# Optimization experiments

Hardware: AMD Instinct MI355X
Metric: run time of the kernel (lower is better)

The kernel has to match this reference:

```python
import jax, jax.numpy as jnp
import numpy as np


def _simple_rnn(x_tbd, Wx, Wh, b, return_sequences):
    # x_tbd: [T, B, D]; h_t = tanh(x_t @ Wx + h_{t-1} @ Wh + b)
    B = x_tbd.shape[1]
    H = Wh.shape[0]
    # precompute input projection for all steps (single big GEMM)
    xw = jnp.einsum('tbd,dh->tbh', x_tbd, Wx) + b

    def step(h, xw_t):
        h_new = jnp.tanh(xw_t + h @ Wh)
        return h_new, h_new if return_sequences else None

    h0 = jnp.zeros((B, H), dtype=x_tbd.dtype)
    h_last, hs = jax.lax.scan(step, h0, xw)
    return hs if return_sequences else h_last


def setup_inputs() -> dict:
    key = jax.random.key(0)
    ks = jax.random.split(key, 8)
    B, T, D, H, C = 32, 1024, 128, 512, 10
    s_in = 1.0 / np.sqrt(D)
    s_h = 1.0 / np.sqrt(H)
    return {
        'x': jax.random.normal(ks[0], (B, T, D), jnp.float32),
        'Wx1': jax.random.normal(ks[1], (D, H), jnp.float32) * s_in,
        'Wh1': jax.random.normal(ks[2], (H, H), jnp.float32) * s_h,
        'b1': jnp.zeros((H,), jnp.float32),
        'Wx2': jax.random.normal(ks[3], (H, H), jnp.float32) * s_h,
        'Wh2': jax.random.normal(ks[4], (H, H), jnp.float32) * s_h,
        'b2': jnp.zeros((H,), jnp.float32),
        'Wo': jax.random.normal(ks[5], (H, C), jnp.float32) * s_h,
        'bo': jnp.zeros((C,), jnp.float32),
    }


def reference(x, Wx1, Wh1, b1, Wx2, Wh2, b2, Wo, bo):
    # x: [B, T, D] -> time-major [T, B, D]
    x_t = jnp.swapaxes(x, 0, 1)
    h1 = _simple_rnn(x_t, Wx1, Wh1, b1, return_sequences=True)   # [T, B, H]
    h2 = _simple_rnn(h1, Wx2, Wh2, b2, return_sequences=False)   # [B, H]
    logits = h2 @ Wo + bo
    return jax.nn.softmax(logits, axis=-1)
```

## Files before the change

### kernel.cpp

```cpp
#include <hip/hip_runtime.h>
#include <hip/hip_fp16.h>
#include <math.h>

#define BATCH 32
#define TLEN  1024
#define DIN   128
#define HID   512
#define NCLS  10
#define NB    2
#define NGRP  (BATCH/NB)
#define NSL   8
#define RING  32
#define SENTV 0xFFFFFFFFu
#define POLL_CAP (1u<<17)

typedef _Float16 hf2 __attribute__((ext_vector_type(2)));

__device__ __forceinline__ unsigned aload(const unsigned* p) {
  return __hip_atomic_load(p, __ATOMIC_RELAXED, __HIP_MEMORY_SCOPE_AGENT);
}
__device__ __forceinline__ void astore(unsigned* p, unsigned v) {
  __hip_atomic_store(p, v, __ATOMIC_RELAXED, __HIP_MEMORY_SCOPE_AGENT);
}
__device__ __forceinline__ int aloadi(const int* p) {
  return __hip_atomic_load(p, __ATOMIC_RELAXED, __HIP_MEMORY_SCOPE_AGENT);
}
__device__ __forceinline__ void astorei(int* p, int v) {
  __hip_atomic_store(p, v, __ATOMIC_RELAXED, __HIP_MEMORY_SCOPE_AGENT);
}

__device__ __forceinline__ float fdot2u(unsigned a, unsigned b, float c) {
#if __has_builtin(__builtin_amdgcn_fdot2)
  return __builtin_amdgcn_fdot2(__builtin_bit_cast(hf2, a),
                                __builtin_bit_cast(hf2, b), c, false);
#else
  hf2 av = __builtin_bit_cast(hf2, a), bv = __builtin_bit_cast(hf2, b);
  return c + (float)av[0] * (float)bv[0] + (float)av[1] * (float)bv[1];
#endif
}

__device__ __forceinline__ unsigned packh2(float lo, float hi) {
  __half2 h = __floats2half2_rn(lo, hi);
  return __builtin_bit_cast(unsigned, h);
}

__global__ __launch_bounds__(256) void k_xw1(
    const float* __restrict__ x, const float* __restrict__ Wx1,
    const float* __restrict__ b1, unsigned* __restrict__ xw1)
{
  __shared__ float xst[DIN * 4];
  const int tid  = threadIdx.x;
  const int row0 = blockIdx.x * 4;
  for (int idx = tid; idx < 4 * DIN; idx += 256) {
    int r = idx >> 7, d = idx & (DIN - 1);
    int row = row0 + r;
    int t = row >> 5, b = row & 31;
    xst[d * 4 + r] = x[((size_t)b * TLEN + t) * DIN + d];
  }
  __syncthreads();
  float acc[4][2];
#pragma unroll
  for (int r = 0; r < 4; ++r) { acc[r][0] = 0.f; acc[r][1] = 0.f; }
  const int j0 = 2 * tid, j1 = 2 * tid + 1;
  for (int d = 0; d < DIN; ++d) {
    float w0 = Wx1[(size_t)d * HID + j0];
    float w1 = Wx1[(size_t)d * HID + j1];
    float4 xv = *reinterpret_cast<const float4*>(&xst[d * 4]);
    acc[0][0] += xv.x * w0; acc[0][1] += xv.x * w1;
    acc[1][0] += xv.y * w0; acc[1][1] += xv.y * w1;
    acc[2][0] += xv.z * w0; acc[2][1] += xv.z * w1;
    acc[3][0] += xv.w * w0; acc[3][1] += xv.w * w1;
  }
  float bb0 = b1[j0], bb1 = b1[j1];
#pragma unroll
  for (int r = 0; r < 4; ++r)
    xw1[(size_t)(row0 + r) * 256 + tid] = packh2(acc[r][0] + bb0, acc[r][1] + bb1);
}

__global__ __launch_bounds__(512, 2) void k_rnn(
    const unsigned* __restrict__ xw1,
    const float* __restrict__ Wh1,
    const float* __restrict__ Wx2, const float* __restrict__ Wh2,
    const float* __restrict__ b2,
    unsigned* __restrict__ ringA,
    unsigned* __restrict__ ringB,
    unsigned* __restrict__ ringC,
    int* __restrict__ prog2,
    float* __restrict__ h2fin)
{
  const int tid  = threadIdx.x;
  const int wgid = blockIdx.x;
  const int layer = wgid >> 7;
  const int lw = wgid & 127;
  const int g  = lw >> 3, sl = lw & 7;
  const int b0 = g * NB;
  const int c0 = sl * 64;
  const int w  = tid >> 6, j = tid & 63;
  const int col = c0 + j;

  __shared__ __align__(16) unsigned h_s[NB][512];
  __shared__ float red[8][NB][64];

  if (layer == 0) {
    const int kw = w * 32;
    unsigned wreg[32];
    {
      const int k0 = w * 64;
#pragma unroll
      for (int i = 0; i < 32; ++i) {
        float a = Wh1[(size_t)(k0 + 2 * i) * HID + col];
        float b = Wh1[(size_t)(k0 + 2 * i + 1) * HID + col];
        wreg[i] = packh2(a, b);
      }
    }
    int cached = -1;
    const int pb = tid >> 8;
    const int pw = tid & 255;
    for (int t = 0; t < TLEN; ++t) {
      unsigned xww = 0;
      if (tid < 128) {
        int bb = tid >> 6, jj = tid & 63;
        xww = xw1[((size_t)t * BATCH + b0 + bb) * 256 + ((c0 + jj) >> 1)];
      }
      if (w < 2) {
        int need = t - (RING - 6);
        if (cached < need) {
          unsigned it = 0;
          for (;;) {
            int p = (j < NSL) ? aloadi(&prog2[g * NSL + j]) : 0x7fffffff;
#pragma unroll
            for (int d = 1; d < NSL; d <<= 1) p = min(p, __shfl_xor(p, d));
            p = __shfl(p, 0);
            cached = p;
            if (cached >= need || ++it >= POLL_CAP) break;
          }
        }
      }
      {
        unsigned v = 0;
        if (t > 0) {
          const unsigned* p =
              &ringA[((size_t)((t - 1) & (RING - 1)) * BATCH + b0 + pb) * 256 + pw];
          unsigned it = 0;
          do { v = aload(p); } while (v == SENTV && ++it < POLL_CAP);
          if (v == SENTV) v = 0;
        }
        h_s[pb][pw] = v;
      }
      if (tid < 64) {
        int bb = tid >> 5, wi = (c0 >> 1) + (tid & 31);
        size_t off = ((size_t)((t + 1) & (RING - 1)) * BATCH + b0 + bb) * 256 + wi;
        astore(&ringA[off], SENTV);
        astore(&ringB[off], SENTV);
      }
      __syncthreads();
      float acc0 = 0.f, acc1 = 0.f;
#pragma unroll
      for (int i = 0; i < 8; ++i) {
        uint4 ha = *reinterpret_cast<const uint4*>(&h_s[0][kw + 4 * i]);
        uint4 hb = *reinterpret_cast<const uint4*>(&h_s[1][kw + 4 * i]);
        acc0 = fdot2u(ha.x, wreg[4 * i + 0], acc0);
        acc0 = fdot2u(ha.y, wreg[4 * i + 1], acc0);
        acc0 = fdot2u(ha.z, wreg[4 * i + 2], acc0);
        acc0 = fdot2u(ha.w, wreg[4 * i + 3], acc0);
        acc1 = fdot2u(hb.x, wreg[4 * i + 0], acc1);
        acc1 = fdot2u(hb.y, wreg[4 * i + 1], acc1);
        acc1 = fdot2u(hb.z, wreg[4 * i + 2], acc1);
        acc1 = fdot2u(hb.w, wreg[4 * i + 3], acc1);
      }
      red[w][0][j] = acc0;
      red[w][1][j] = acc1;
      __syncthreads();
      if (tid < 128) {
        int bb = tid >> 6, jj = tid & 63;
        hf2 xv = __builtin_bit_cast(hf2, xww);
        float z = (float)xv[jj & 1];
#pragma unroll
        for (int r = 0; r < 8; ++r) z += red[r][bb][jj];
        float h = tanhf(z);
        float hn = __shfl_down(h, 1);
        if ((jj & 1) == 0) {
          unsigned u = packh2(h, hn);
          size_t off = ((size_t)(t & (RING - 1)) * BATCH + b0 + bb) * 256 + ((c0 + jj) >> 1);
          astore(&ringA[off], u);
          astore(&ringB[off], u);
        }
      }
    }
  } else {
    const int kw = w * 64;
    unsigned wreg[64];
    {
      const int k0 = w * 128;
#pragma unroll
      for (int i = 0; i < 64; ++i) {
        int k = k0 + 2 * i;
        float a, b;
        if (k < HID) {
          a = Wx2[(size_t)k * HID + col];
          b = Wx2[(size_t)(k + 1) * HID + col];
        } else {
          a = Wh2[(size_t)(k - HID) * HID + col];
          b = Wh2[(size_t)(k - HID + 1) * HID + col];
        }
        wreg[i] = packh2(a, b);
      }
    }
    float b2v = 0.f;
    if (tid < 128) b2v = b2[c0 + (tid & 63)];
    for (int t = 0; t < TLEN; ++t) {
      {
        const unsigned* p0 = nullptr; const unsigned* p1 = nullptr;
        unsigned v0 = 0, v1 = 0;
        if (tid < 256) {
          size_t base = ((size_t)(t & (RING - 1)) * BATCH + b0) * 256 + tid;
          p0 = &ringB[base]; p1 = &ringB[base + 256];
          v0 = SENTV; v1 = SENTV;
        } else if (t > 0) {
          size_t base = ((size_t)((t - 1) & (RING - 1)) * BATCH + b0) * 256 + (tid - 256);
          p0 = &ringC[base]; p1 = &ringC[base + 256];
          v0 = SENTV; v1 = SENTV;
        }
        if (p0) {
          unsigned it = 0;
          while ((v0 == SENTV || v1 == SENTV) && it < POLL_CAP) {
            if (v0 == SENTV) v0 = aload(p0);
            if (v1 == SENTV) v1 = aload(p1);
            ++it;
          }
          if (v0 == SENTV) v0 = 0;
          if (v1 == SENTV) v1 = 0;
        }
        h_s[0][tid] = v0;
        h_s[1][tid] = v1;
      }
      if (tid < 64) {
        int bb = tid >> 5, wi = (c0 >> 1) + (tid & 31);
        astore(&ringC[((size_t)((t + 1) & (RING - 1)) * BATCH + b0 + bb) * 256 + wi], SENTV);
      }
      __syncthreads();
      if (tid == 0) astorei(&prog2[g * NSL + sl], t);
      float acc0 = 0.f, acc1 = 0.f;
#pragma unroll
      for (int i = 0; i < 16; ++i) {
        uint4 ha = *reinterpret_cast<const uint4*>(&h_s[0][kw + 4 * i]);
        uint4 hb = *reinterpret_cast<const uint4*>(&h_s[1][kw + 4 * i]);
        acc0 = fdot2u(ha.x, wreg[4 * i + 0], acc0);
        acc0 = fdot2u(ha.y, wreg[4 * i + 1], acc0);
        acc0 = fdot2u(ha.z, wreg[4 * i + 2], acc0);
        acc0 = fdot2u(ha.w, wreg[4 * i + 3], acc0);
        acc1 = fdot2u(hb.x, wreg[4 * i + 0], acc1);
        acc1 = fdot2u(hb.y, wreg[4 * i + 1], acc1);
        acc1 = fdot2u(hb.z, wreg[4 * i + 2], acc1);
        acc1 = fdot2u(hb.w, wreg[4 * i + 3], acc1);
      }
      red[w][0][j] = acc0;
      red[w][1][j] = acc1;
      __syncthreads();
      if (tid < 128) {
        int bb = tid >> 6, jj = tid & 63;
        float z = b2v;
#pragma unroll
        for (int r = 0; r < 8; ++r) z += red[r][bb][jj];
        float h = tanhf(z);
        if (t == TLEN - 1) h2fin[(size_t)(b0 + bb) * HID + c0 + jj] = h;
        float hn = __shfl_down(h, 1);
        if ((jj & 1) == 0) {
          astore(&ringC[((size_t)(t & (RING - 1)) * BATCH + b0 + bb) * 256 + ((c0 + jj) >> 1)],
                 packh2(h, hn));
        }
      }
    }
  }
}

__global__ __launch_bounds__(640) void k_head(
    const float* __restrict__ h2, const float* __restrict__ Wo,
    const float* __restrict__ bo, float* __restrict__ out)
{
  __shared__ float lg[16];
  const int b = blockIdx.x;
  const int c = threadIdx.x >> 6;
  const int l = threadIdx.x & 63;
  float p = 0.f;
#pragma unroll
  for (int i = 0; i < 8; ++i) {
    int k = l + 64 * i;
    p += h2[(size_t)b * HID + k] * Wo[(size_t)k * NCLS + c];
  }
  for (int off = 32; off; off >>= 1) p += __shfl_down(p, off);
  if (l == 0) lg[c] = p + bo[c];
  __syncthreads();
  if (threadIdx.x == 0) {
    float m = lg[0];
    for (int i = 1; i < NCLS; ++i) m = fmaxf(m, lg[i]);
    float e[NCLS];
    float s = 0.f;
    for (int i = 0; i < NCLS; ++i) { e[i] = expf(lg[i] - m); s += e[i]; }
    for (int i = 0; i < NCLS; ++i) out[(size_t)b * NCLS + i] = e[i] / s;
  }
}

extern "C" void kernel_launch(void* const* d_in, const int* in_sizes, int n_in,
                              void* d_out, int out_size, void* d_ws, size_t ws_size,
                              hipStream_t stream)
{
  (void)in_sizes; (void)n_in; (void)out_size; (void)ws_size;
  const float* x   = (const float*)d_in[0];
  const float* Wx1 = (const float*)d_in[1];
  const float* Wh1 = (const float*)d_in[2];
  const float* b1  = (const float*)d_in[3];
  const float* Wx2 = (const float*)d_in[4];
  const float* Wh2 = (const float*)d_in[5];
  const float* b2  = (const float*)d_in[6];
  const float* Wo  = (const float*)d_in[7];
  const float* bo  = (const float*)d_in[8];
  float* out = (float*)d_out;

  char* ws = (char*)d_ws;
  size_t o = 0;
  unsigned* xw1 = (unsigned*)(ws + o); o += (size_t)TLEN * BATCH * 256 * 4;
  const size_t ringBytes = (size_t)RING * BATCH * 256 * 4;
  unsigned* ringA = (unsigned*)(ws + o); o += ringBytes;
  unsigned* ringB = (unsigned*)(ws + o); o += ringBytes;
  unsigned* ringC = (unsigned*)(ws + o); o += ringBytes;
  int* prog2 = (int*)(ws + o); o += 1024;
  float* h2fin = (float*)(ws + o); o += (size_t)BATCH * HID * 4;

  hipMemsetAsync(ringA, 0xFF, 3 * ringBytes, stream);
  hipMemsetAsync(prog2, 0xFF, NGRP * NSL * 4, stream);

  k_xw1<<<TLEN * BATCH / 4, 256, 0, stream>>>(x, Wx1, b1, xw1);
  k_rnn<<<256, 512, 0, stream>>>(xw1, Wh1, Wx2, Wh2, b2,
                                 ringA, ringB, ringC, prog2, h2fin);
  k_head<<<BATCH, 640, 0, stream>>>(h2fin, Wo, bo, out);
}
```

Baseline: 2.445 ms.

## Reduce partial sums via wave shuffles and double-buffer shared hidden state

Each wave now owns 16 output columns of one batch row. Four lane-quarters split the K dimension and are combined with cross-lane shuffles, which removes the shared-memory reduction array and the second barrier per timestep. The shared hidden-state buffer is double-buffered by step parity so one barrier per step is enough. The duplicate layer-1 ring is merged into one buffer read by both layers. Weight registers per thread double, and the occupancy hint in the launch bounds is dropped, which raises register pressure.

```diff
diff --git a/kernel.cpp b/kernel.cpp
--- a/kernel.cpp
+++ b/kernel.cpp
@@ -77,13 +77,12 @@
     xw1[(size_t)(row0 + r) * 256 + tid] = packh2(acc[r][0] + bb0, acc[r][1] + bb1);
 }
 
-__global__ __launch_bounds__(512, 2) void k_rnn(
+__global__ __launch_bounds__(512) void k_rnn(
     const unsigned* __restrict__ xw1,
     const float* __restrict__ Wh1,
     const float* __restrict__ Wx2, const float* __restrict__ Wh2,
     const float* __restrict__ b2,
-    unsigned* __restrict__ ringA,
-    unsigned* __restrict__ ringB,
+    unsigned* __restrict__ ring1,
     unsigned* __restrict__ ringC,
     int* __restrict__ prog2,
     float* __restrict__ h2fin)
@@ -95,180 +94,152 @@
   const int g  = lw >> 3, sl = lw & 7;
   const int b0 = g * NB;
   const int c0 = sl * 64;
-  const int w  = tid >> 6, j = tid & 63;
-  const int col = c0 + j;
-
-  __shared__ __align__(16) unsigned h_s[NB][512];
-  __shared__ float red[8][NB][64];
+  const int w  = tid >> 6, l = tid & 63;
+  const int q  = l >> 4;
+  const int lo = l & 15;
+  const int o  = w * 16 + lo;
+  const int obb = o >> 6, oj = o & 63;
+  const int ocol = c0 + oj;
+
+  const int pw = tid & 255;
+  const int pb = tid >> 8;
+
+  __shared__ __align__(16) unsigned h_s[2][NB][512];
 
   if (layer == 0) {
-    const int kw = w * 32;
-    unsigned wreg[32];
+    unsigned wreg[64];
     {
-      const int k0 = w * 64;
-#pragma unroll
-      for (int i = 0; i < 32; ++i) {
-        float a = Wh1[(size_t)(k0 + 2 * i) * HID + col];
-        float b = Wh1[(size_t)(k0 + 2 * i + 1) * HID + col];
+      const int k0 = q * 128;
+#pragma unroll
+      for (int i = 0; i < 64; ++i) {
+        float a = Wh1[(size_t)(k0 + 2 * i) * HID + ocol];
+        float b = Wh1[(size_t)(k0 + 2 * i + 1) * HID + ocol];
         wreg[i] = packh2(a, b);
       }
     }
     int cached = -1;
-    const int pb = tid >> 8;
-    const int pw = tid & 255;
     for (int t = 0; t < TLEN; ++t) {
+      const int p = t & 1;
       unsigned xww = 0;
-      if (tid < 128) {
-        int bb = tid >> 6, jj = tid & 63;
-        xww = xw1[((size_t)t * BATCH + b0 + bb) * 256 + ((c0 + jj) >> 1)];
-      }
-      if (w < 2) {
-        int need = t - (RING - 6);
+      if (q == 0)
+        xww = xw1[((size_t)t * BATCH + b0 + obb) * 256 + (ocol >> 1)];
+      if (w == 0) {
+        const int need = t - (RING - 6);
         if (cached < need) {
           unsigned it = 0;
           for (;;) {
-            int p = (j < NSL) ? aloadi(&prog2[g * NSL + j]) : 0x7fffffff;
-#pragma unroll
-            for (int d = 1; d < NSL; d <<= 1) p = min(p, __shfl_xor(p, d));
-            p = __shfl(p, 0);
-            cached = p;
+            int pr = (l < NSL) ? aloadi(&prog2[g * NSL + l]) : 0x7fffffff;
+#pragma unroll
+            for (int d = 1; d < NSL; d <<= 1) pr = min(pr, __shfl_xor(pr, d));
+            pr = __shfl(pr, 0);
+            cached = pr;
             if (cached >= need || ++it >= POLL_CAP) break;
           }
         }
+        int rb = l >> 5, rw = (c0 >> 1) + (l & 31);
+        astore(&ring1[((size_t)((t + 1) & (RING - 1)) * BATCH + b0 + rb) * 256 + rw], SENTV);
       }
       {
         unsigned v = 0;
         if (t > 0) {
-          const unsigned* p =
-              &ringA[((size_t)((t - 1) & (RING - 1)) * BATCH + b0 + pb) * 256 + pw];
+          const unsigned* pp =
+              &ring1[((size_t)((t - 1) & (RING - 1)) * BATCH + b0 + pb) * 256 + pw];
           unsigned it = 0;
-          do { v = aload(p); } while (v == SENTV && ++it < POLL_CAP);
+          do { v = aload(pp); } while (v == SENTV && ++it < POLL_CAP);
           if (v == SENTV) v = 0;
         }
-        h_s[pb][pw] = v;
-      }
-      if (tid < 64) {
-        int bb = tid >> 5, wi = (c0 >> 1) + (tid & 31);
-        size_t off = ((size_t)((t + 1) & (RING - 1)) * BATCH + b0 + bb) * 256 + wi;
-        astore(&ringA[off], SENTV);
-        astore(&ringB[off], SENTV);
+        h_s[p][pb][pw] = v;
       }
       __syncthreads();
-      float acc0 = 0.f, acc1 = 0.f;
-#pragma unroll
-      for (int i = 0; i < 8; ++i) {
-        uint4 ha = *reinterpret_cast<const uint4*>(&h_s[0][kw + 4 * i]);
-        uint4 hb = *reinterpret_cast<const uint4*>(&h_s[1][kw + 4 * i]);
-        acc0 = fdot2u(ha.x, wreg[4 * i + 0], acc0);
-        acc0 = fdot2u(ha.y, wreg[4 * i + 1], acc0);
-        acc0 = fdot2u(ha.z, wreg[4 * i + 2], acc0);
-        acc0 = fdot2u(ha.w, wreg[4 * i + 3], acc0);
-        acc1 = fdot2u(hb.x, wreg[4 * i + 0], acc1);
-        acc1 = fdot2u(hb.y, wreg[4 * i + 1], acc1);
-        acc1 = fdot2u(hb.z, wreg[4 * i + 2], acc1);
-        acc1 = fdot2u(hb.w, wreg[4 * i + 3], acc1);
-      }
-      red[w][0][j] = acc0;
-      red[w][1][j] = acc1;
-      __syncthreads();
-      if (tid < 128) {
-        int bb = tid >> 6, jj = tid & 63;
+      float acc = 0.f;
+      const unsigned* hp = &h_s[p][obb][q * 64];
+#pragma unroll
+      for (int i = 0; i < 16; ++i) {
+        uint4 hv = *reinterpret_cast<const uint4*>(&hp[4 * i]);
+        acc = fdot2u(hv.x, wreg[4 * i + 0], acc);
+        acc = fdot2u(hv.y, wreg[4 * i + 1], acc);
+        acc = fdot2u(hv.z, wreg[4 * i + 2], acc);
+        acc = fdot2u(hv.w, wreg[4 * i + 3], acc);
+      }
+      acc += __shfl_xor(acc, 16);
+      acc += __shfl_xor(acc, 32);
+      if (q == 0) {
         hf2 xv = __builtin_bit_cast(hf2, xww);
-        float z = (float)xv[jj & 1];
-#pragma unroll
-        for (int r = 0; r < 8; ++r) z += red[r][bb][jj];
+        float z = (float)xv[oj & 1] + acc;
         float h = tanhf(z);
         float hn = __shfl_down(h, 1);
-        if ((jj & 1) == 0) {
-          unsigned u = packh2(h, hn);
-          size_t off = ((size_t)(t & (RING - 1)) * BATCH + b0 + bb) * 256 + ((c0 + jj) >> 1);
-          astore(&ringA[off], u);
-          astore(&ringB[off], u);
-        }
+        if (!(lo & 1))
+          astore(&ring1[((size_t)(t & (RING - 1)) * BATCH + b0 + obb) * 256 + (ocol >> 1)],
+                 packh2(h, hn));
       }
     }
   } else {
-    const int kw = w * 64;
-    unsigned wreg[64];
+    unsigned wreg[128];
     {
-      const int k0 = w * 128;
-#pragma unroll
-      for (int i = 0; i < 64; ++i) {
+      const int k0 = q * 256;
+#pragma unroll
+      for (int i = 0; i < 128; ++i) {
         int k = k0 + 2 * i;
         float a, b;
         if (k < HID) {
-          a = Wx2[(size_t)k * HID + col];
-          b = Wx2[(size_t)(k + 1) * HID + col];
+          a = Wx2[(size_t)k * HID + ocol];
+          b = Wx2[(size_t)(k + 1) * HID + ocol];
         } else {
-          a = Wh2[(size_t)(k - HID) * HID + col];
-          b = Wh2[(size_t)(k - HID + 1) * HID + col];
+          a = Wh2[(size_t)(k - HID) * HID + ocol];
+          b = Wh2[(size_t)(k - HID + 1) * HID + ocol];
         }
         wreg[i] = packh2(a, b);
       }
     }
-    float b2v = 0.f;
-    if (tid < 128) b2v = b2[c0 + (tid & 63)];
+    float b2v = (q == 0) ? b2[ocol] : 0.f;
     for (int t = 0; t < TLEN; ++t) {
+      const int p = t & 1;
       {
-        const unsigned* p0 = nullptr; const unsigned* p1 = nullptr;
-        unsigned v0 = 0, v1 = 0;
-        if (tid < 256) {
-          size_t base = ((size_t)(t & (RING - 1)) * BATCH + b0) * 256 + tid;
-          p0 = &ringB[base]; p1 = &ringB[base + 256];
-          v0 = SENTV; v1 = SENTV;
-        } else if (t > 0) {
-          size_t base = ((size_t)((t - 1) & (RING - 1)) * BATCH + b0) * 256 + (tid - 256);
-          p0 = &ringC[base]; p1 = &ringC[base + 256];
-          v0 = SENTV; v1 = SENTV;
+        const unsigned* p0 =
+            &ring1[((size_t)(t & (RING - 1)) * BATCH + b0 + pb) * 256 + pw];
+        unsigned v0 = SENTV, v1 = SENTV;
+        const unsigned* p1 = nullptr;
+        if (t > 0)
+          p1 = &ringC[((size_t)((t - 1) & (RING - 1)) * BATCH + b0 + pb) * 256 + pw];
+        else
+          v1 = 0;
+        unsigned it = 0;
+        while ((v0 == SENTV || v1 == SENTV) && it < POLL_CAP) {
+          if (v0 == SENTV) v0 = aload(p0);
+          if (v1 == SENTV && p1) v1 = aload(p1);
+          ++it;
         }
-        if (p0) {
-          unsigned it = 0;
-          while ((v0 == SENTV || v1 == SENTV) && it < POLL_CAP) {
-            if (v0 == SENTV) v0 = aload(p0);
-            if (v1 == SENTV) v1 = aload(p1);
-            ++it;
-          }
-          if (v0 == SENTV) v0 = 0;
-          if (v1 == SENTV) v1 = 0;
-        }
-        h_s[0][tid] = v0;
-        h_s[1][tid] = v1;
-      }
-      if (tid < 64) {
-        int bb = tid >> 5, wi = (c0 >> 1) + (tid & 31);
-        astore(&ringC[((size_t)((t + 1) & (RING - 1)) * BATCH + b0 + bb) * 256 + wi], SENTV);
+        if (v0 == SENTV) v0 = 0;
+        if (v1 == SENTV) v1 = 0;
+        h_s[p][pb][pw] = v0;
+        h_s[p][pb][256 + pw] = v1;
+      }
+      if (w == 0) {
+        int rb = l >> 5, rw = (c0 >> 1) + (l & 31);
+        astore(&ringC[((size_t)((t + 1) & (RING - 1)) * BATCH + b0 + rb) * 256 + rw], SENTV);
       }
       __syncthreads();
       if (tid == 0) astorei(&prog2[g * NSL + sl], t);
-      float acc0 = 0.f, acc1 = 0.f;
-#pragma unroll
-      for (int i = 0; i < 16; ++i) {
-        uint4 ha = *reinterpret_cast<const uint4*>(&h_s[0][kw + 4 * i]);
-        uint4 hb = *reinterpret_cast<const uint4*>(&h_s[1][kw + 4 * i]);
-        acc0 = fdot2u(ha.x, wreg[4 * i + 0], acc0);
-        acc0 = fdot2u(ha.y, wreg[4 * i + 1], acc0);
-        acc0 = fdot2u(ha.z, wreg[4 * i + 2], acc0);
-        acc0 = fdot2u(ha.w, wreg[4 * i + 3], acc0);
-        acc1 = fdot2u(hb.x, wreg[4 * i + 0], acc1);
-        acc1 = fdot2u(hb.y, wreg[4 * i + 1], acc1);
-        acc1 = fdot2u(hb.z, wreg[4 * i + 2], acc1);
-        acc1 = fdot2u(hb.w, wreg[4 * i + 3], acc1);
-      }
-      red[w][0][j] = acc0;
-      red[w][1][j] = acc1;
-      __syncthreads();
-      if (tid < 128) {
-        int bb = tid >> 6, jj = tid & 63;
-        float z = b2v;
-#pragma unroll
-        for (int r = 0; r < 8; ++r) z += red[r][bb][jj];
+      float acc = 0.f;
+      const unsigned* hp = &h_s[p][obb][q * 128];
+#pragma unroll
+      for (int i = 0; i < 32; ++i) {
+        uint4 hv = *reinterpret_cast<const uint4*>(&hp[4 * i]);
+        acc = fdot2u(hv.x, wreg[4 * i + 0], acc);
+        acc = fdot2u(hv.y, wreg[4 * i + 1], acc);
+        acc = fdot2u(hv.z, wreg[4 * i + 2], acc);
+        acc = fdot2u(hv.w, wreg[4 * i + 3], acc);
+      }
+      acc += __shfl_xor(acc, 16);
+      acc += __shfl_xor(acc, 32);
+      if (q == 0) {
+        float z = b2v + acc;
         float h = tanhf(z);
-        if (t == TLEN - 1) h2fin[(size_t)(b0 + bb) * HID + c0 + jj] = h;
+        if (t == TLEN - 1) h2fin[(size_t)(b0 + obb) * HID + ocol] = h;
         float hn = __shfl_down(h, 1);
-        if ((jj & 1) == 0) {
-          astore(&ringC[((size_t)(t & (RING - 1)) * BATCH + b0 + bb) * 256 + ((c0 + jj) >> 1)],
+        if (!(lo & 1))
+          astore(&ringC[((size_t)(t & (RING - 1)) * BATCH + b0 + obb) * 256 + (ocol >> 1)],
                  packh2(h, hn));
-        }
       }
     }
   }
@@ -321,17 +292,16 @@
   size_t o = 0;
   unsigned* xw1 = (unsigned*)(ws + o); o += (size_t)TLEN * BATCH * 256 * 4;
   const size_t ringBytes = (size_t)RING * BATCH * 256 * 4;
-  unsigned* ringA = (unsigned*)(ws + o); o += ringBytes;
-  unsigned* ringB = (unsigned*)(ws + o); o += ringBytes;
+  unsigned* ring1 = (unsigned*)(ws + o); o += ringBytes;
   unsigned* ringC = (unsigned*)(ws + o); o += ringBytes;
   int* prog2 = (int*)(ws + o); o += 1024;
   float* h2fin = (float*)(ws + o); o += (size_t)BATCH * HID * 4;
 
-  hipMemsetAsync(ringA, 0xFF, 3 * ringBytes, stream);
+  hipMemsetAsync(ring1, 0xFF, 2 * ringBytes, stream);
   hipMemsetAsync(prog2, 0xFF, NGRP * NSL * 4, stream);
 
   k_xw1<<<TLEN * BATCH / 4, 256, 0, stream>>>(x, Wx1, b1, xw1);
   k_rnn<<<256, 512, 0, stream>>>(xw1, Wh1, Wx2, Wh2, b2,
-                                 ringA, ringB, ringC, prog2, h2fin);
+                                 ring1, ringC, prog2, h2fin);
   k_head<<<BATCH, 640, 0, stream>>>(h2fin, Wo, bo, out);
 }
```

New measurement: 2.355 ms. -3.7%, faster.
